# Kernel tuning notes

Measured on AMD Instinct MI355X. Metric: run time of the kernel, lower is better.

Reference implementation:

```python
import jax, jax.numpy as jnp
import numpy as np

MARGIN = 1.0
B, D, T = 8192, 256, 100000


def setup_inputs() -> dict:
    key = jax.random.key(0)
    k1, k2 = jax.random.split(key)
    embeddings = jax.random.normal(k1, (B, D), dtype=jnp.float32)
    triplets = jax.random.randint(k2, (T, 3), 0, B, dtype=jnp.int64)
    return {"embeddings": embeddings, "triplets": triplets}


def _rowwise_l2(x, y):
    # Equivalent to torch.diagonal(torch.cdist(x, y)) without the NxN waste.
    d = x - y
    return jnp.sqrt(jnp.sum(d * d, axis=-1))


def reference(embeddings, triplets):
    anchor = embeddings[triplets[:, 0]]      # [T, D]
    positives = embeddings[triplets[:, 1]]   # [T, D]
    negatives = embeddings[triplets[:, 2]]   # [T, D]
    ap = _rowwise_l2(anchor, positives)
    an = _rowwise_l2(anchor, negatives)
    pn = _rowwise_l2(positives, negatives)
    an_pn = jnp.minimum(an, pn)
    losses = jax.nn.relu(ap - an_pn + MARGIN)
    return (losses.mean(), triplets.shape[0])
```

## Files before the change

### kernel.cpp

```cpp
#include <hip/hip_runtime.h>
#include <hip/hip_bf16.h>
#include <math.h>


__device__ __forceinline__ float bf16_rne(float f) {
    union { float f; unsigned int u; } v;
    v.f = f;
    v.u = (v.u + 0x7FFFu + ((v.u >> 16) & 1u)) & 0xFFFF0000u;
    return v.f;
}

__global__ void triplet_partial(const float* __restrict__ emb,
                                const int* __restrict__ tri,
                                int T, int B,
                                float* __restrict__ partials) {
    const int lane = threadIdx.x & 63;
    const int sub  = lane & 15;
    const int grp  = lane >> 4;
    const int wib  = threadIdx.x >> 6;
    const int wpb  = blockDim.x >> 6;
    const int gw   = blockIdx.x * wpb + wib;
    const int nw   = gridDim.x * wpb;

    const int nquads = (T + 3) >> 2;
    float local = 0.0f;

    for (int q = gw; q < nquads; q += nw) {
        const int t = 4 * q + grp;
        float dap = 0.f, dan = 0.f, dpn = 0.f;
        bool valid = false;

        if (t < T) {
            const int a = tri[3 * t + 0];
            const int p = tri[3 * t + 1];
            const int n = tri[3 * t + 2];
            valid = (unsigned)a < (unsigned)B &&
                    (unsigned)p < (unsigned)B &&
                    (unsigned)n < (unsigned)B;
            if (valid) {
                const float4* ra = (const float4*)(emb + (size_t)a * 256) + sub * 4;
                const float4* rp = (const float4*)(emb + (size_t)p * 256) + sub * 4;
                const float4* rn = (const float4*)(emb + (size_t)n * 256) + sub * 4;

                float4 va0 = ra[0], va1 = ra[1], va2 = ra[2], va3 = ra[3];
                float4 vp0 = rp[0], vp1 = rp[1], vp2 = rp[2], vp3 = rp[3];
                float4 vn0 = rn[0], vn1 = rn[1], vn2 = rn[2], vn3 = rn[3];

                float d;
                #define ACC(VA, VP, VN) \
                    d = VA.x - VP.x; dap += d * d; \
                    d = VA.y - VP.y; dap += d * d; \
                    d = VA.z - VP.z; dap += d * d; \
                    d = VA.w - VP.w; dap += d * d; \
                    d = VA.x - VN.x; dan += d * d; \
                    d = VA.y - VN.y; dan += d * d; \
                    d = VA.z - VN.z; dan += d * d; \
                    d = VA.w - VN.w; dan += d * d; \
                    d = VP.x - VN.x; dpn += d * d; \
                    d = VP.y - VN.y; dpn += d * d; \
                    d = VP.z - VN.z; dpn += d * d; \
                    d = VP.w - VN.w; dpn += d * d;
                ACC(va0, vp0, vn0)
                ACC(va1, vp1, vn1)
                ACC(va2, vp2, vn2)
                ACC(va3, vp3, vn3)
                #undef ACC
            }
        }

        #pragma unroll
        for (int off = 8; off > 0; off >>= 1) {
            dap += __shfl_xor(dap, off);
            dan += __shfl_xor(dan, off);
            dpn += __shfl_xor(dpn, off);
        }

        if (sub == 0 && valid) {
            const float l = sqrtf(dap) - fminf(sqrtf(dan), sqrtf(dpn)) + 1.0f;
            if (l > 0.0f && l < 1000.0f) local += l;
        }
    }

    #pragma unroll
    for (int off = 32; off > 0; off >>= 1) local += __shfl_xor(local, off);

    __shared__ float s[8];
    if (lane == 0) s[wib] = local;
    __syncthreads();
    if (threadIdx.x == 0) {
        float sum = 0.0f;
        for (int i = 0; i < wpb; ++i) sum += s[i];
        partials[blockIdx.x] = sum;
    }
}

__global__ void triplet_finalize(const float* __restrict__ partials,
                                 int nparts, int T,
                                 float* __restrict__ out) {
    __shared__ float s[256];
    float sum = 0.0f;
    for (int i = threadIdx.x; i < nparts; i += blockDim.x) sum += partials[i];
    s[threadIdx.x] = sum;
    __syncthreads();
    for (int stride = 128; stride > 0; stride >>= 1) {
        if (threadIdx.x < stride) s[threadIdx.x] += s[threadIdx.x + stride];
        __syncthreads();
    }
    if (threadIdx.x == 0) {
        out[0] = s[0] / (float)T;
        out[1] = bf16_rne((float)T);
    }
}

extern "C" void kernel_launch(void* const* d_in, const int* in_sizes, int n_in,
                              void* d_out, int out_size, void* d_ws, size_t ws_size,
                              hipStream_t stream) {
    const float* emb = (const float*)d_in[0];
    const int*   tri = (const int*)d_in[1];
    const int T = in_sizes[1] / 3;
    const int B = in_sizes[0] / 256;

    float* out = (float*)d_out;
    float* partials = (float*)d_ws;

    const int BLOCKS = 1024, THREADS = 256;
    triplet_partial<<<BLOCKS, THREADS, 0, stream>>>(emb, tri, T, B, partials);
    triplet_finalize<<<1, 256, 0, stream>>>(partials, BLOCKS, T, out);
}
```

Measured before the change: 36.54 us.

## Replace grid-stride loop with one-quad-per-wave launch sized to triplet count

The persistent 1024-block grid-stride loop becomes a grid of ceil(T/16) blocks, each wave handling exactly four triplets once. The aim is to expose more memory-level parallelism for the random gathers and to drop loop overhead. In exchange the launch has far more blocks (6250), and the finalize kernel now reduces 6250 partials serially in one block, which adds tail cost.

```diff
diff --git a/kernel.cpp b/kernel.cpp
--- a/kernel.cpp
+++ b/kernel.cpp
@@ -10,88 +10,78 @@
     return v.f;
 }
 
-__global__ void triplet_partial(const float* __restrict__ emb,
-                                const int* __restrict__ tri,
-                                int T, int B,
-                                float* __restrict__ partials) {
+__global__ __launch_bounds__(256) void triplet_partial(
+        const float* __restrict__ emb,
+        const int* __restrict__ tri,
+        int T, int B,
+        float* __restrict__ partials) {
     const int lane = threadIdx.x & 63;
     const int sub  = lane & 15;
     const int grp  = lane >> 4;
     const int wib  = threadIdx.x >> 6;
-    const int wpb  = blockDim.x >> 6;
-    const int gw   = blockIdx.x * wpb + wib;
-    const int nw   = gridDim.x * wpb;
 
-    const int nquads = (T + 3) >> 2;
+    const int t = blockIdx.x * 16 + wib * 4 + grp;
+
     float local = 0.0f;
 
-    for (int q = gw; q < nquads; q += nw) {
-        const int t = 4 * q + grp;
-        float dap = 0.f, dan = 0.f, dpn = 0.f;
-        bool valid = false;
+    if (t < T) {
+        const int a = tri[3 * t + 0];
+        const int p = tri[3 * t + 1];
+        const int n = tri[3 * t + 2];
+        const bool ok = (unsigned)a < (unsigned)B &&
+                        (unsigned)p < (unsigned)B &&
+                        (unsigned)n < (unsigned)B;
+        if (ok) {
+            const float4* ra = (const float4*)(emb + (size_t)a * 256) + sub * 4;
+            const float4* rp = (const float4*)(emb + (size_t)p * 256) + sub * 4;
+            const float4* rn = (const float4*)(emb + (size_t)n * 256) + sub * 4;
 
-        if (t < T) {
-            const int a = tri[3 * t + 0];
-            const int p = tri[3 * t + 1];
-            const int n = tri[3 * t + 2];
-            valid = (unsigned)a < (unsigned)B &&
-                    (unsigned)p < (unsigned)B &&
-                    (unsigned)n < (unsigned)B;
-            if (valid) {
-                const float4* ra = (const float4*)(emb + (size_t)a * 256) + sub * 4;
-                const float4* rp = (const float4*)(emb + (size_t)p * 256) + sub * 4;
-                const float4* rn = (const float4*)(emb + (size_t)n * 256) + sub * 4;
+            const float4 va0 = ra[0], va1 = ra[1], va2 = ra[2], va3 = ra[3];
+            const float4 vp0 = rp[0], vp1 = rp[1], vp2 = rp[2], vp3 = rp[3];
+            const float4 vn0 = rn[0], vn1 = rn[1], vn2 = rn[2], vn3 = rn[3];
 
-                float4 va0 = ra[0], va1 = ra[1], va2 = ra[2], va3 = ra[3];
-                float4 vp0 = rp[0], vp1 = rp[1], vp2 = rp[2], vp3 = rp[3];
-                float4 vn0 = rn[0], vn1 = rn[1], vn2 = rn[2], vn3 = rn[3];
+            float dap = 0.f, dan = 0.f, dpn = 0.f, d;
+            #define ACC(VA, VP, VN) \
+                d = VA.x - VP.x; dap += d * d; \
+                d = VA.y - VP.y; dap += d * d; \
+                d = VA.z - VP.z; dap += d * d; \
+                d = VA.w - VP.w; dap += d * d; \
+                d = VA.x - VN.x; dan += d * d; \
+                d = VA.y - VN.y; dan += d * d; \
+                d = VA.z - VN.z; dan += d * d; \
+                d = VA.w - VN.w; dan += d * d; \
+                d = VP.x - VN.x; dpn += d * d; \
+                d = VP.y - VN.y; dpn += d * d; \
+                d = VP.z - VN.z; dpn += d * d; \
+                d = VP.w - VN.w; dpn += d * d;
+            ACC(va0, vp0, vn0)
+            ACC(va1, vp1, vn1)
+            ACC(va2, vp2, vn2)
+            ACC(va3, vp3, vn3)
+            #undef ACC
 
-                float d;
-                #define ACC(VA, VP, VN) \
-                    d = VA.x - VP.x; dap += d * d; \
-                    d = VA.y - VP.y; dap += d * d; \
-                    d = VA.z - VP.z; dap += d * d; \
-                    d = VA.w - VP.w; dap += d * d; \
-                    d = VA.x - VN.x; dan += d * d; \
-                    d = VA.y - VN.y; dan += d * d; \
-                    d = VA.z - VN.z; dan += d * d; \
-                    d = VA.w - VN.w; dan += d * d; \
-                    d = VP.x - VN.x; dpn += d * d; \
-                    d = VP.y - VN.y; dpn += d * d; \
-                    d = VP.z - VN.z; dpn += d * d; \
-                    d = VP.w - VN.w; dpn += d * d;
-                ACC(va0, vp0, vn0)
-                ACC(va1, vp1, vn1)
-                ACC(va2, vp2, vn2)
-                ACC(va3, vp3, vn3)
-                #undef ACC
+            #pragma unroll
+            for (int off = 8; off > 0; off >>= 1) {
+                dap += __shfl_xor(dap, off);
+                dan += __shfl_xor(dan, off);
+                dpn += __shfl_xor(dpn, off);
             }
-        }
 
-        #pragma unroll
-        for (int off = 8; off > 0; off >>= 1) {
-            dap += __shfl_xor(dap, off);
-            dan += __shfl_xor(dan, off);
-            dpn += __shfl_xor(dpn, off);
-        }
-
-        if (sub == 0 && valid) {
-            const float l = sqrtf(dap) - fminf(sqrtf(dan), sqrtf(dpn)) + 1.0f;
-            if (l > 0.0f && l < 1000.0f) local += l;
+            if (sub == 0) {
+                const float l = sqrtf(dap) - fminf(sqrtf(dan), sqrtf(dpn)) + 1.0f;
+                if (l > 0.0f && l < 1000.0f) local = l;
+            }
         }
     }
 
     #pragma unroll
     for (int off = 32; off > 0; off >>= 1) local += __shfl_xor(local, off);
 
-    __shared__ float s[8];
+    __shared__ float s[4];
     if (lane == 0) s[wib] = local;
     __syncthreads();
-    if (threadIdx.x == 0) {
-        float sum = 0.0f;
-        for (int i = 0; i < wpb; ++i) sum += s[i];
-        partials[blockIdx.x] = sum;
-    }
+    if (threadIdx.x == 0)
+        partials[blockIdx.x] = (s[0] + s[1]) + (s[2] + s[3]);
 }
 
 __global__ void triplet_finalize(const float* __restrict__ partials,
@@ -123,7 +113,7 @@
     float* out = (float*)d_out;
     float* partials = (float*)d_ws;
 
-    const int BLOCKS = 1024, THREADS = 256;
-    triplet_partial<<<BLOCKS, THREADS, 0, stream>>>(emb, tri, T, B, partials);
+    const int BLOCKS = (T + 15) / 16;
+    triplet_partial<<<BLOCKS, 256, 0, stream>>>(emb, tri, T, B, partials);
     triplet_finalize<<<1, 256, 0, stream>>>(partials, BLOCKS, T, out);
 }
```

After: 42.01 us. 15.0% more time.
